# Kernel optimization log

Hardware: AMD Instinct MI355X
Metric: run time of the kernel (lower is better)

Reference implementation:

```python
import jax, jax.numpy as jnp
import numpy as np

PI = 3.141592653589793
IMG = 256           # img_size (input_resolution)
CONV = 2 * IMG      # conv_size for linear convolution
PITCH = 6.4e-6      # feature_size (m)
WAVELENGTH = 5.2e-7 # green channel, wavelength_list[1]
DISTANCE = 0.2      # distance_list[1] (m)
SCALE_OUT = 0.95    # scale_output


def make_H(n, pitch, wl, z):
    """Angular-spectrum transfer function, unshifted (fft) frequency order."""
    fx = np.fft.fftfreq(n, d=pitch).astype(np.float64)
    FX, FY = np.meshgrid(fx, fx, indexing='xy')
    fz2 = (1.0 / wl) ** 2 - FX ** 2 - FY ** 2
    prop = fz2 > 0
    kz = 2.0 * np.pi * np.sqrt(np.maximum(fz2, 0.0))
    H = np.exp(1j * kz * z) * prop
    return jnp.asarray(H.astype(np.complex64))


def setup_inputs() -> dict:
    key = jax.random.key(0)
    k1, k2, k3 = jax.random.split(key, 3)
    K, D = 512, 256
    z_e_x = jax.random.normal(k1, (16, D, 64, 64), dtype=jnp.float32)
    poh_dec = jax.random.normal(k2, (16, 1, IMG, IMG), dtype=jnp.float32)
    emb = jax.random.uniform(k3, (K, D), dtype=jnp.float32,
                             minval=-1.0 / K, maxval=1.0 / K)
    H = make_H(CONV, PITCH, WAVELENGTH, DISTANCE)
    return {"z_e_x": z_e_x, "poh_dec": poh_dec, "emb": emb, "H": H}


def vq_straight_through(z_e_x, emb):
    # z_e_x: [B, D, h, w] -> BHWC flatten [N, D]
    B, D, h, w = z_e_x.shape
    ze = jnp.transpose(z_e_x, (0, 2, 3, 1)).reshape(-1, D)
    # squared L2 distances to codebook [N, K]
    d2 = (jnp.sum(ze * ze, axis=1, keepdims=True)
          - 2.0 * ze @ emb.T
          + jnp.sum(emb * emb, axis=1))
    idx = jnp.argmin(d2, axis=1)                      # [N]
    zq = jnp.take(emb, idx, axis=0).reshape(B, h, w, D)
    z_q_x = jnp.transpose(zq, (0, 3, 1, 2))           # BCHW (grads -> emb)
    # straight-through: codebook detached, grad flows to z_e_x
    z_q_x_st = z_e_x + jax.lax.stop_gradient(z_q_x - z_e_x)
    return z_q_x_st, z_q_x


def recon_hologram(poh, H):
    # unit-amplitude phase-only field: exp(i*poh)
    field = jax.lax.complex(jnp.cos(poh), jnp.sin(poh))
    pad = (CONV - IMG) // 2
    padded = jnp.pad(field, ((0, 0), (0, 0), (pad, pad), (pad, pad)))  # zero pad
    u = jnp.fft.fft2(jnp.fft.ifftshift(padded, axes=(-2, -1)), norm='ortho')
    u = H * u
    u = jnp.fft.fftshift(jnp.fft.ifft2(u, norm='ortho'), axes=(-2, -1))
    u = u[..., pad:pad + IMG, pad:pad + IMG]          # center crop
    intensity = (jnp.abs(u) ** 2) * SCALE_OUT
    return jnp.sqrt(intensity)


def reference(z_e_x, poh_dec, emb, H):
    z_q_x_st, z_q_x = vq_straight_through(z_e_x, emb)
    # decoder (external VQGAN blocks) stands in as poh_dec; then Hardtanh(-pi, pi)
    poh = jnp.clip(poh_dec, -PI, PI)
    recon_img = recon_hologram(poh, H)
    return (poh, recon_img, z_e_x, z_q_x)
```

## Files before the change

kernel.cpp:

```cpp
#include <hip/hip_runtime.h>

#define PI_F 3.14159265358979323846f

typedef __attribute__((ext_vector_type(8))) _Float16 f16x8;
typedef __attribute__((ext_vector_type(4))) _Float16 f16x4;
typedef __attribute__((ext_vector_type(4))) float floatx4;
typedef __attribute__((ext_vector_type(4))) float f32x4;
typedef __attribute__((ext_vector_type(2))) float f32x2;

__device__ __forceinline__ void gload16(const void* src, void* dst) {
    __builtin_amdgcn_global_load_lds(
        (const __attribute__((address_space(1))) unsigned int*)src,
        (__attribute__((address_space(3))) unsigned int*)dst, 16, 0, 0);
}

__device__ __forceinline__ f32x4 ntload4(const float* p) {
    return __builtin_nontemporal_load((const f32x4*)p);
}
__device__ __forceinline__ void ntstore4(float* p, f32x4 v) {
    __builtin_nontemporal_store(v, (f32x4*)p);
}
__device__ __forceinline__ float2 ntload2(const float2* p) {
    return __builtin_bit_cast(float2, __builtin_nontemporal_load((const f32x2*)p));
}
__device__ __forceinline__ void ntstore2(float2* p, float2 v) {
    __builtin_nontemporal_store(__builtin_bit_cast(f32x2, v), (f32x2*)p);
}
__device__ __forceinline__ float ntload1(const float* p) {
    return __builtin_nontemporal_load(p);
}
__device__ __forceinline__ void ntstore1(float* p, float v) {
    __builtin_nontemporal_store(v, p);
}

__device__ __forceinline__ int swz(int p) { return p ^ ((p >> 5) & 15); }

__device__ __forceinline__ float2 cadd(float2 a, float2 b) {
    return make_float2(a.x + b.x, a.y + b.y);
}
__device__ __forceinline__ float2 csub(float2 a, float2 b) {
    return make_float2(a.x - b.x, a.y - b.y);
}
__device__ __forceinline__ float2 cmul(float2 a, float2 w) {
    return make_float2(a.x * w.x - a.y * w.y, a.x * w.y + a.y * w.x);
}
__device__ __forceinline__ float2 cmulc(float2 a, float2 w) {
    return make_float2(a.x * w.x + a.y * w.y, a.y * w.x - a.x * w.y);
}

template <int S>
__device__ __forceinline__ void dif_triple(float2* X, const float2* tw, int ss) {
    const int Q = 1 << (S - 2);
    int block = ss >> (S - 2);
    int j0 = ss & (Q - 1);
    int base = (block << (S + 1)) + j0;
    float2 v[8];
#pragma unroll
    for (int t = 0; t < 8; ++t) v[t] = X[swz(base + t * Q)];
#pragma unroll
    for (int t = 0; t < 4; ++t) {
        float2 w = tw[(j0 + t * Q) << (8 - S)];
        float2 a = v[t], b = v[t + 4];
        v[t] = cadd(a, b);
        v[t + 4] = cmul(csub(a, b), w);
    }
#pragma unroll
    for (int h = 0; h < 2; ++h)
#pragma unroll
        for (int t0 = 0; t0 < 2; ++t0) {
            int t = h * 4 + t0;
            float2 w = tw[(j0 + t0 * Q) << (9 - S)];
            float2 a = v[t], b = v[t + 2];
            v[t] = cadd(a, b);
            v[t + 2] = cmul(csub(a, b), w);
        }
    {
        float2 w = tw[j0 << (10 - S)];
#pragma unroll
        for (int t = 0; t < 8; t += 2) {
            float2 a = v[t], b = v[t + 1];
            v[t] = cadd(a, b);
            v[t + 1] = cmul(csub(a, b), w);
        }
    }
#pragma unroll
    for (int t = 0; t < 8; ++t) X[swz(base + t * Q)] = v[t];
}

template <int S>
__device__ __forceinline__ void dit_triple(float2* X, const float2* tw, int ss) {
    const int Q = 1 << (S - 2);
    int block = ss >> (S - 2);
    int j0 = ss & (Q - 1);
    int base = (block << (S + 1)) + j0;
    float2 v[8];
#pragma unroll
    for (int t = 0; t < 8; ++t) v[t] = X[swz(base + t * Q)];
    {
        float2 w = tw[j0 << (10 - S)];
#pragma unroll
        for (int t = 0; t < 8; t += 2) {
            float2 a = v[t], b = cmulc(v[t + 1], w);
            v[t] = cadd(a, b);
            v[t + 1] = csub(a, b);
        }
    }
#pragma unroll
    for (int h = 0; h < 2; ++h)
#pragma unroll
        for (int t0 = 0; t0 < 2; ++t0) {
            int t = h * 4 + t0;
            float2 w = tw[(j0 + t0 * Q) << (9 - S)];
            float2 a = v[t], b = cmulc(v[t + 2], w);
            v[t] = cadd(a, b);
            v[t + 2] = csub(a, b);
        }
#pragma unroll
    for (int t = 0; t < 4; ++t) {
        float2 w = tw[(j0 + t * Q) << (8 - S)];
        float2 a = v[t], b = cmulc(v[t + 4], w);
        v[t] = cadd(a, b);
        v[t + 4] = csub(a, b);
    }
#pragma unroll
    for (int t = 0; t < 8; ++t) X[swz(base + t * Q)] = v[t];
}

__global__ void k_init(float2* __restrict__ Hs, const float* __restrict__ emb,
                       _Float16* __restrict__ eh, float* __restrict__ eq) {
    __shared__ float red[4];
    int blk = blockIdx.x;
    if (blk < 1024) {
        int g = blk * 256 + threadIdx.x;
        int ybr = g >> 9, xbr = g & 511;
        int ky = __brev((unsigned)ybr) >> 23;
        int kx = __brev((unsigned)xbr) >> 23;
        double val = 1.0 / (512.0 * 6.4e-6);
        double fy = (double)((ky < 256) ? ky : ky - 512) * val;
        double fx = (double)((kx < 256) ? kx : kx - 512) * val;
        double iw = 1.0 / 5.2e-7;
        double px = fx * fx, py = fy * fy;
        double fz2 = (iw * iw - px) - py;
        float2 h = make_float2(0.f, 0.f);
        if (fz2 > 0.0) {
            double t = sqrt(fz2) * 0.2;
            double fr = t - floor(t);
            double sv, cv;
            sincospi(2.0 * fr, &sv, &cv);
            const double sc = 1.0 / 262144.0;
            h = make_float2((float)(cv * sc), (float)(sv * sc));
        }
        Hs[g] = h;
    } else {
        int k = blk - 1024;
        int t = threadIdx.x;
        float v = emb[k * 256 + t];
        eh[k * 256 + t] = (_Float16)v;
        float s = v * v;
        for (int off = 32; off; off >>= 1) s += __shfl_down(s, off);
        if ((t & 63) == 0) red[t >> 6] = s;
        __syncthreads();
        if (t == 0) eq[k] = red[0] + red[1] + red[2] + red[3];
    }
}

__global__ __launch_bounds__(256, 3) void k_vq(const float* __restrict__ ze,
                                               const _Float16* __restrict__ eh,
                                               const float* __restrict__ eq,
                                               int* __restrict__ idx,
                                               float* __restrict__ zeout) {
    __shared__ _Float16 B[2][4096];
    __shared__ _Float16 Ast[4][32][136];
    int tid = threadIdx.x;
    int lane = tid & 63, wave = tid >> 6;
    int n0 = blockIdx.x * 128 + wave * 32;
    int b = n0 >> 12;
    int s0 = n0 & 4095;
    int m = lane & 15;
    int q = lane >> 4;

    const _Float16* srcp = eh + m * 256 + (wave * 4 + q) * 8;

#define STAGE(kt_, buf_)  do {                                               \
        const _Float16* s_ = srcp + (kt_) * 4096;    \
        _Float16* d_ = &B[buf_][wave * 512];                                 \
        gload16(s_,       d_);                                               \
        gload16(s_ + 128, d_ + 2048);         \
    } while (0)

    STAGE(0, 0);

    const float* zb = ze + (size_t)b * (256 * 4096);
    float* zo = zeout ? zeout + (size_t)b * (256 * 4096) : nullptr;
    int g = lane >> 3;
    int s4 = lane & 7;
    f16x8 a[2][8];
#pragma unroll
    for (int half = 0; half < 2; ++half) {
#pragma unroll
        for (int c2 = 0; c2 < 4; ++c2) {
            int c = half * 4 + c2;
            float vv[4][4];
#pragma unroll
            for (int dd = 0; dd < 4; ++dd) {
                int d = c * 32 + g * 4 + dd;
                size_t off = (size_t)d * 4096 + s0 + s4 * 4;
                f32x4 t = ntload4(&zb[off]);
                if (zeout) ntstore4(&zo[off], t);
                vv[dd][0] = t.x; vv[dd][1] = t.y;
                vv[dd][2] = t.z; vv[dd][3] = t.w;
            }
#pragma unroll
            for (int i = 0; i < 4; ++i) {
                f16x4 p = {(_Float16)vv[0][i], (_Float16)vv[1][i],
                           (_Float16)vv[2][i], (_Float16)vv[3][i]};
                *(f16x4*)&Ast[wave][s4 * 4 + i][c2 * 32 + g * 4] = p;
            }
        }
#pragma unroll
        for (int c2 = 0; c2 < 4; ++c2)
#pragma unroll
            for (int T = 0; T < 2; ++T)
                a[T][half * 4 + c2] =
                    *(const f16x8*)&Ast[wave][T * 16 + m][c2 * 32 + q * 8];
    }
    __syncthreads();

    float best[2][4];
    int bidx[2][4];
#pragma unroll
    for (int T = 0; T < 2; ++T)
#pragma unroll
        for (int r = 0; r < 4; ++r) { best[T][r] = 3.4e38f; bidx[T][r] = 0x7fffffff; }

    int cur = 0;
    for (int kt = 0; kt < 32; ++kt) {
        if (kt < 31) STAGE(kt + 1, cur ^ 1);

        int kc = kt * 16 + m;
        float eqv = eq[kc];
        floatx4 acc0 = {0.f, 0.f, 0.f, 0.f};
        floatx4 acc1 = {0.f, 0.f, 0.f, 0.f};
        const _Float16* b0 = &B[cur][q * 128 + m * 8];
#pragma unroll
        for (int c = 0; c < 8; ++c) {
            f16x8 bb = *(const f16x8*)(b0 + c * 512);
            acc0 = __builtin_amdgcn_mfma_f32_16x16x32_f16(a[0][c], bb, acc0, 0, 0, 0);
            acc1 = __builtin_amdgcn_mfma_f32_16x16x32_f16(a[1][c], bb, acc1, 0, 0, 0);
        }
#pragma unroll
        for (int r = 0; r < 4; ++r) {
            float d0 = eqv - 2.0f * acc0[r];
            if (d0 < best[0][r]) { best[0][r] = d0; bidx[0][r] = kc; }
            float d1 = eqv - 2.0f * acc1[r];
            if (d1 < best[1][r]) { best[1][r] = d1; bidx[1][r] = kc; }
        }
        __syncthreads();
        cur ^= 1;
    }
#undef STAGE

#pragma unroll
    for (int T = 0; T < 2; ++T)
#pragma unroll
        for (int r = 0; r < 4; ++r) {
            float bv = best[T][r];
            int bi = bidx[T][r];
            for (int off = 1; off < 16; off <<= 1) {
                float ov = __shfl_xor(bv, off);
                int oi = __shfl_xor(bi, off);
                if (ov < bv || (ov == bv && oi < bi)) { bv = ov; bi = oi; }
            }
            if (m == 0) idx[n0 + T * 16 + q * 4 + r] = bi;
        }
}

__global__ __launch_bounds__(256) void k_zq(const float* __restrict__ emb,
                                            const int* __restrict__ idx,
                                            float* __restrict__ out4) {
    __shared__ float E[32 * 257];
    __shared__ int sidx[32];
    int tid = threadIdx.x;
    int blk = blockIdx.x;
    int b = blk >> 7;
    int s0 = (blk & 127) << 5;
    if (tid < 32) sidx[tid] = idx[(b << 12) + s0 + tid];
    __syncthreads();
#pragma unroll
    for (int i = 0; i < 32; ++i)
        E[i * 257 + tid] = emb[sidx[i] * 256 + tid];
    __syncthreads();
    float* ob = out4 + ((size_t)b << 20) + s0;
    int s_off = tid & 31, d0 = tid >> 5;
#pragma unroll
    for (int i2 = 0; i2 < 32; ++i2) {
        int d = d0 + (i2 << 3);
        ntstore1(&ob[((size_t)d << 12) + s_off], E[s_off * 257 + d]);
    }
}

__global__ void k_ze(const float* __restrict__ ze, float* __restrict__ out3) {
    size_t g = (size_t)blockIdx.x * 256 + threadIdx.x;
    ntstore4(&((float*)out3)[g * 4], ntload4(&((const float*)ze)[g * 4]));
}

__global__ __launch_bounds__(256) void k_fwd_rows(const float* __restrict__ poh_in,
                                                  float* __restrict__ poh_out,
                                                  float2* __restrict__ F) {
    __shared__ float2 Xs[4][512];
    __shared__ float2 tw[256];
    int tid = threadIdx.x;
    {
        float sv, cv;
        sincospif(-(float)tid * (1.0f / 256.0f), &sv, &cv);
        tw[tid] = make_float2(cv, sv);
    }
    __syncthreads();
    int wave = tid >> 6, lane = tid & 63;
    int b = blockIdx.x >> 6;
    int t = ((blockIdx.x & 63) << 2) + wave;
    int jy = (t < 128) ? t : t + 256;
    int ry = (t < 128) ? t + 128 : t - 128;
    float2* X = Xs[wave];

    const float* prow = poh_in + (b << 16) + (ry << 8);
    float* orow = poh_out + (b << 16) + (ry << 8);
#pragma unroll
    for (int c0 = 0; c0 < 256; c0 += 64) {
        int c = c0 + lane;
        float v = ntload1(&prow[c]);
        v = fminf(fmaxf(v, -PI_F), PI_F);
        ntstore1(&orow[c], v);
        float sv, cv;
        __sincosf(v, &sv, &cv);
        int jx = (c < 128) ? c + 384 : c - 128;
        X[swz(jx)] = make_float2(cv, sv);
    }
#pragma unroll
    for (int p0 = 128; p0 < 384; p0 += 64) X[swz(p0 + lane)] = make_float2(0.f, 0.f);

    dif_triple<8>(X, tw, lane);
    dif_triple<5>(X, tw, lane);
    dif_triple<2>(X, tw, lane);

    float2* Frow = F + ((size_t)(b * 512 + jy) << 9);
#pragma unroll
    for (int p0 = 0; p0 < 512; p0 += 64)
        ntstore2(&Frow[p0 + lane], X[swz(p0 + lane)]);
}

__global__ __launch_bounds__(256) void k_cols(float2* __restrict__ F,
                                              const float2* __restrict__ Hs) {
    __shared__ float2 X[8 * 514];
    __shared__ float2 tw[256];
    int tid = threadIdx.x;
    {
        float sv, cv;
        sincospif(-(float)tid * (1.0f / 256.0f), &sv, &cv);
        tw[tid] = make_float2(cv, sv);
    }
    int b = blockIdx.x >> 6;
    int jx0 = (blockIdx.x & 63) << 3;
    const size_t ibase = ((size_t)b << 18);

#pragma unroll
    for (int i0 = 0; i0 < 8 * 256; i0 += 256) {
        int ii = i0 + tid;
        int col = ii & 7, rr = ii >> 3;
        int jy = (rr < 128) ? rr : rr + 256;
        X[col * 514 + swz(jy)] = ntload2(&F[ibase + ((size_t)jy << 9) + jx0 + col]);
    }
#pragma unroll
    for (int i0 = 0; i0 < 8 * 256; i0 += 256) {
        int ii = i0 + tid;
        int col = ii & 7, rr = ii >> 3;
        X[col * 514 + swz(128 + rr)] = make_float2(0.f, 0.f);
    }
    __syncthreads();

    int wave = tid >> 6, lane = tid & 63;
    int colh = lane >> 5;
    int r = lane & 31;
    float2* Xc = X + (wave * 2 + colh) * 514;

    dif_triple<8>(Xc, tw, r);       dif_triple<8>(Xc, tw, 32 + r);
    dif_triple<5>(Xc, tw, r);       dif_triple<5>(Xc, tw, 32 + r);
    dif_triple<2>(Xc, tw, r);       dif_triple<2>(Xc, tw, 32 + r);

    {
        int gc = jx0 + wave * 2 + colh;
#pragma unroll
        for (int p0 = 0; p0 < 512; p0 += 32) {
            int p = p0 + r;
            float2 h = Hs[((size_t)p << 9) + gc];
            int qs = swz(p);
            Xc[qs] = cmul(Xc[qs], h);
        }
    }

    dit_triple<2>(Xc, tw, r);       dit_triple<2>(Xc, tw, 32 + r);
    dit_triple<5>(Xc, tw, r);       dit_triple<5>(Xc, tw, 32 + r);
    dit_triple<8>(Xc, tw, r);       dit_triple<8>(Xc, tw, 32 + r);

    __syncthreads();
#pragma unroll
    for (int i0 = 0; i0 < 8 * 256; i0 += 256) {
        int ii = i0 + tid;
        int col = ii & 7, rr = ii >> 3;
        int jy = (rr < 128) ? rr : rr + 256;
        ntstore2(&F[ibase + ((size_t)jy << 9) + jx0 + col],
                 X[col * 514 + swz(jy)]);
    }
}

__global__ __launch_bounds__(256) void k_inv_rows(const float2* __restrict__ F,
                                                  float* __restrict__ out2) {
    __shared__ float2 Xs[4][512];
    __shared__ float2 tw[256];
    int tid = threadIdx.x;
    {
        float sv, cv;
        sincospif(-(float)tid * (1.0f / 256.0f), &sv, &cv);
        tw[tid] = make_float2(cv, sv);
    }
    __syncthreads();
    int wave = tid >> 6, lane = tid & 63;
    int b = blockIdx.x >> 6;
    int t = ((blockIdx.x & 63) << 2) + wave;
    int jy = (t < 128) ? t : t + 256;
    int r = (t < 128) ? t + 128 : t - 128;
    float2* X = Xs[wave];

    const float2* Frow = F + ((size_t)(b * 512 + jy) << 9);
#pragma unroll
    for (int p0 = 0; p0 < 512; p0 += 64)
        X[swz(p0 + lane)] = ntload2(&Frow[p0 + lane]);

    dit_triple<2>(X, tw, lane);
    dit_triple<5>(X, tw, lane);
    dit_triple<8>(X, tw, lane);

    float* orow = out2 + (b << 16) + (r << 8);
    const float SC = 0.97467943448f;
#pragma unroll
    for (int c0 = 0; c0 < 256; c0 += 64) {
        int c = c0 + lane;
        int jx = (c < 128) ? c + 384 : c - 128;
        float2 u = X[swz(jx)];
        ntstore1(&orow[c], sqrtf(u.x * u.x + u.y * u.y) * SC);
    }
}

extern "C" void kernel_launch(void* const* d_in, const int* in_sizes, int n_in,
                              void* d_out, int out_size, void* d_ws, size_t ws_size,
                              hipStream_t stream) {
    const float* ze  = (const float*)d_in[0];
    const float* poh = (const float*)d_in[1];
    const float* emb = (const float*)d_in[2];

    float* out  = (float*)d_out;
    float* out1 = out;
    float* out2 = out + 1048576;
    float* out3 = out + 2097152;
    float* out4 = out + 18874368;

    const size_t WS_NEED = 262144 + 2048 + 262144 + 2097152;
    bool fused = (d_ws != nullptr) && (ws_size >= WS_NEED);
    char* base = fused ? (char*)d_ws : (char*)out3;
    _Float16* eh;
    float* eq;
    int* idxp;
    float2* Hs;
    if (fused) {
        eh   = (_Float16*)base;
        eq   = (float*)(base + 262144);
        idxp = (int*)(base + 264192);
        Hs   = (float2*)(base + 526336);
    } else {
        eh   = (_Float16*)base;
        eq   = (float*)(base + 262144);
        idxp = (int*)(base + 264192);
        Hs   = (float2*)(base + 1048576);
    }
    float2* F = (float2*)out4;

    k_init    <<<1536, 256, 0, stream>>>(Hs, emb, eh, eq);
    k_vq      <<<512, 256, 0, stream>>>(ze, eh, eq, idxp,
                                        fused ? out3 : (float*)nullptr);
    k_fwd_rows<<<1024, 256, 0, stream>>>(poh, out1, F);
    k_cols    <<<1024, 256, 0, stream>>>(F, Hs);
    k_inv_rows<<<1024, 256, 0, stream>>>(F, out2);
    k_zq      <<<2048, 256, 0, stream>>>(emb, idxp, out4);
    if (!fused)
        k_ze  <<<16384, 256, 0, stream>>>(ze, out3);
}
```

Before: 265.5 us.

## Merge VQ argmin and forward row FFT into one heterogeneous launch

Combines the VQ nearest-codebook kernel and the forward row FFT kernel into a single launch whose blocks branch by blockIdx: the first 512 blocks do VQ and the remaining 1024 do the row FFTs, sharing one raw shared-memory buffer. The intent is to run the MFMA-bound VQ work alongside the memory-bound FFT rows and to drop one kernel launch and its tail. The cost is that every block reserves the larger shared-memory footprint and the launch bounds of the VQ path, which may lower occupancy for the FFT blocks.

```diff
diff --git a/kernel.cpp b/kernel.cpp
--- a/kernel.cpp
+++ b/kernel.cpp
@@ -164,115 +164,162 @@
     }
 }
 
-__global__ __launch_bounds__(256, 3) void k_vq(const float* __restrict__ ze,
-                                               const _Float16* __restrict__ eh,
-                                               const float* __restrict__ eq,
-                                               int* __restrict__ idx,
-                                               float* __restrict__ zeout) {
-    __shared__ _Float16 B[2][4096];
-    __shared__ _Float16 Ast[4][32][136];
+__global__ __launch_bounds__(256, 3) void k_vq_fwd(
+        const float* __restrict__ ze, const _Float16* __restrict__ eh,
+        const float* __restrict__ eq, int* __restrict__ idx,
+        float* __restrict__ zeout,
+        const float* __restrict__ poh_in, float* __restrict__ poh_out,
+        float2* __restrict__ F) {
+    __shared__ __align__(16) char smem[51200];
     int tid = threadIdx.x;
     int lane = tid & 63, wave = tid >> 6;
-    int n0 = blockIdx.x * 128 + wave * 32;
-    int b = n0 >> 12;
-    int s0 = n0 & 4095;
-    int m = lane & 15;
-    int q = lane >> 4;
-
-    const _Float16* srcp = eh + m * 256 + (wave * 4 + q) * 8;
+
+    if (blockIdx.x < 512) {
+        _Float16* B = (_Float16*)smem;
+        _Float16* Ast = (_Float16*)(smem + 16384);
+        int n0 = blockIdx.x * 128 + wave * 32;
+        int b = n0 >> 12;
+        int s0 = n0 & 4095;
+        int m = lane & 15;
+        int q = lane >> 4;
+
+        const _Float16* srcp = eh + m * 256 + (wave * 4 + q) * 8;
 
 #define STAGE(kt_, buf_)  do {                                               \
         const _Float16* s_ = srcp + (kt_) * 4096;    \
-        _Float16* d_ = &B[buf_][wave * 512];                                 \
+        _Float16* d_ = B + (buf_) * 4096 + wave * 512;                       \
         gload16(s_,       d_);                                               \
         gload16(s_ + 128, d_ + 2048);         \
     } while (0)
 
-    STAGE(0, 0);
-
-    const float* zb = ze + (size_t)b * (256 * 4096);
-    float* zo = zeout ? zeout + (size_t)b * (256 * 4096) : nullptr;
-    int g = lane >> 3;
-    int s4 = lane & 7;
-    f16x8 a[2][8];
-#pragma unroll
-    for (int half = 0; half < 2; ++half) {
-#pragma unroll
-        for (int c2 = 0; c2 < 4; ++c2) {
-            int c = half * 4 + c2;
-            float vv[4][4];
-#pragma unroll
-            for (int dd = 0; dd < 4; ++dd) {
-                int d = c * 32 + g * 4 + dd;
-                size_t off = (size_t)d * 4096 + s0 + s4 * 4;
-                f32x4 t = ntload4(&zb[off]);
-                if (zeout) ntstore4(&zo[off], t);
-                vv[dd][0] = t.x; vv[dd][1] = t.y;
-                vv[dd][2] = t.z; vv[dd][3] = t.w;
+        STAGE(0, 0);
+
+        const float* zb = ze + (size_t)b * (256 * 4096);
+        float* zo = zeout ? zeout + (size_t)b * (256 * 4096) : nullptr;
+        int g = lane >> 3;
+        int s4 = lane & 7;
+        _Float16* Aw = Ast + wave * (32 * 136);
+        f16x8 a[2][8];
+#pragma unroll
+        for (int half = 0; half < 2; ++half) {
+#pragma unroll
+            for (int c2 = 0; c2 < 4; ++c2) {
+                int c = half * 4 + c2;
+                float vv[4][4];
+#pragma unroll
+                for (int dd = 0; dd < 4; ++dd) {
+                    int d = c * 32 + g * 4 + dd;
+                    size_t off = (size_t)d * 4096 + s0 + s4 * 4;
+                    f32x4 t = ntload4(&zb[off]);
+                    if (zeout) ntstore4(&zo[off], t);
+                    vv[dd][0] = t.x; vv[dd][1] = t.y;
+                    vv[dd][2] = t.z; vv[dd][3] = t.w;
+                }
+#pragma unroll
+                for (int i = 0; i < 4; ++i) {
+                    f16x4 p = {(_Float16)vv[0][i], (_Float16)vv[1][i],
+                               (_Float16)vv[2][i], (_Float16)vv[3][i]};
+                    *(f16x4*)&Aw[(s4 * 4 + i) * 136 + c2 * 32 + g * 4] = p;
+                }
             }
 #pragma unroll
-            for (int i = 0; i < 4; ++i) {
-                f16x4 p = {(_Float16)vv[0][i], (_Float16)vv[1][i],
-                           (_Float16)vv[2][i], (_Float16)vv[3][i]};
-                *(f16x4*)&Ast[wave][s4 * 4 + i][c2 * 32 + g * 4] = p;
+            for (int c2 = 0; c2 < 4; ++c2)
+#pragma unroll
+                for (int T = 0; T < 2; ++T)
+                    a[T][half * 4 + c2] =
+                        *(const f16x8*)&Aw[(T * 16 + m) * 136 + c2 * 32 + q * 8];
+        }
+        __syncthreads();
+
+        float best[2][4];
+        int bidx[2][4];
+#pragma unroll
+        for (int T = 0; T < 2; ++T)
+#pragma unroll
+            for (int r = 0; r < 4; ++r) { best[T][r] = 3.4e38f; bidx[T][r] = 0x7fffffff; }
+
+        int cur = 0;
+        for (int kt = 0; kt < 32; ++kt) {
+            if (kt < 31) STAGE(kt + 1, cur ^ 1);
+
+            int kc = kt * 16 + m;
+            float eqv = eq[kc];
+            floatx4 acc0 = {0.f, 0.f, 0.f, 0.f};
+            floatx4 acc1 = {0.f, 0.f, 0.f, 0.f};
+            const _Float16* b0 = B + cur * 4096 + q * 128 + m * 8;
+#pragma unroll
+            for (int c = 0; c < 8; ++c) {
+                f16x8 bb = *(const f16x8*)(b0 + c * 512);
+                acc0 = __builtin_amdgcn_mfma_f32_16x16x32_f16(a[0][c], bb, acc0, 0, 0, 0);
+                acc1 = __builtin_amdgcn_mfma_f32_16x16x32_f16(a[1][c], bb, acc1, 0, 0, 0);
             }
-        }
-#pragma unroll
-        for (int c2 = 0; c2 < 4; ++c2)
-#pragma unroll
-            for (int T = 0; T < 2; ++T)
-                a[T][half * 4 + c2] =
-                    *(const f16x8*)&Ast[wave][T * 16 + m][c2 * 32 + q * 8];
-    }
-    __syncthreads();
-
-    float best[2][4];
-    int bidx[2][4];
-#pragma unroll
-    for (int T = 0; T < 2; ++T)
-#pragma unroll
-        for (int r = 0; r < 4; ++r) { best[T][r] = 3.4e38f; bidx[T][r] = 0x7fffffff; }
-
-    int cur = 0;
-    for (int kt = 0; kt < 32; ++kt) {
-        if (kt < 31) STAGE(kt + 1, cur ^ 1);
-
-        int kc = kt * 16 + m;
-        float eqv = eq[kc];
-        floatx4 acc0 = {0.f, 0.f, 0.f, 0.f};
-        floatx4 acc1 = {0.f, 0.f, 0.f, 0.f};
-        const _Float16* b0 = &B[cur][q * 128 + m * 8];
-#pragma unroll
-        for (int c = 0; c < 8; ++c) {
-            f16x8 bb = *(const f16x8*)(b0 + c * 512);
-            acc0 = __builtin_amdgcn_mfma_f32_16x16x32_f16(a[0][c], bb, acc0, 0, 0, 0);
-            acc1 = __builtin_amdgcn_mfma_f32_16x16x32_f16(a[1][c], bb, acc1, 0, 0, 0);
-        }
-#pragma unroll
-        for (int r = 0; r < 4; ++r) {
-            float d0 = eqv - 2.0f * acc0[r];
-            if (d0 < best[0][r]) { best[0][r] = d0; bidx[0][r] = kc; }
-            float d1 = eqv - 2.0f * acc1[r];
-            if (d1 < best[1][r]) { best[1][r] = d1; bidx[1][r] = kc; }
+#pragma unroll
+            for (int r = 0; r < 4; ++r) {
+                float d0 = eqv - 2.0f * acc0[r];
+                if (d0 < best[0][r]) { best[0][r] = d0; bidx[0][r] = kc; }
+                float d1 = eqv - 2.0f * acc1[r];
+                if (d1 < best[1][r]) { best[1][r] = d1; bidx[1][r] = kc; }
+            }
+            __syncthreads();
+            cur ^= 1;
+        }
+#undef STAGE
+
+#pragma unroll
+        for (int T = 0; T < 2; ++T)
+#pragma unroll
+            for (int r = 0; r < 4; ++r) {
+                float bv = best[T][r];
+                int bi = bidx[T][r];
+                for (int off = 1; off < 16; off <<= 1) {
+                    float ov = __shfl_xor(bv, off);
+                    int oi = __shfl_xor(bi, off);
+                    if (ov < bv || (ov == bv && oi < bi)) { bv = ov; bi = oi; }
+                }
+                if (m == 0) idx[n0 + T * 16 + q * 4 + r] = bi;
+            }
+    } else {
+        float2* Xs = (float2*)smem;
+        float2* tw = (float2*)(smem + 16384);
+        int blk = blockIdx.x - 512;
+        {
+            float sv, cv;
+            sincospif(-(float)tid * (1.0f / 256.0f), &sv, &cv);
+            tw[tid] = make_float2(cv, sv);
         }
         __syncthreads();
-        cur ^= 1;
-    }
-#undef STAGE
-
-#pragma unroll
-    for (int T = 0; T < 2; ++T)
-#pragma unroll
-        for (int r = 0; r < 4; ++r) {
-            float bv = best[T][r];
-            int bi = bidx[T][r];
-            for (int off = 1; off < 16; off <<= 1) {
-                float ov = __shfl_xor(bv, off);
-                int oi = __shfl_xor(bi, off);
-                if (ov < bv || (ov == bv && oi < bi)) { bv = ov; bi = oi; }
-            }
-            if (m == 0) idx[n0 + T * 16 + q * 4 + r] = bi;
-        }
+        int b = blk >> 6;
+        int t = ((blk & 63) << 2) + wave;
+        int jy = (t < 128) ? t : t + 256;
+        int ry = (t < 128) ? t + 128 : t - 128;
+        float2* X = Xs + wave * 512;
+
+        const float* prow = poh_in + (b << 16) + (ry << 8);
+        float* orow = poh_out + (b << 16) + (ry << 8);
+#pragma unroll
+        for (int c0 = 0; c0 < 256; c0 += 64) {
+            int c = c0 + lane;
+            float v = ntload1(&prow[c]);
+            v = fminf(fmaxf(v, -PI_F), PI_F);
+            ntstore1(&orow[c], v);
+            float sv, cv;
+            __sincosf(v, &sv, &cv);
+            int jx = (c < 128) ? c + 384 : c - 128;
+            X[swz(jx)] = make_float2(cv, sv);
+        }
+#pragma unroll
+        for (int p0 = 128; p0 < 384; p0 += 64)
+            X[swz(p0 + lane)] = make_float2(0.f, 0.f);
+
+        dif_triple<8>(X, tw, lane);
+        dif_triple<5>(X, tw, lane);
+        dif_triple<2>(X, tw, lane);
+
+        float2* Frow = F + ((size_t)(b * 512 + jy) << 9);
+#pragma unroll
+        for (int p0 = 0; p0 < 512; p0 += 64)
+            ntstore2(&Frow[p0 + lane], X[swz(p0 + lane)]);
+    }
 }
 
 __global__ __launch_bounds__(256) void k_zq(const float* __restrict__ emb,
@@ -302,51 +349,6 @@
 __global__ void k_ze(const float* __restrict__ ze, float* __restrict__ out3) {
     size_t g = (size_t)blockIdx.x * 256 + threadIdx.x;
     ntstore4(&((float*)out3)[g * 4], ntload4(&((const float*)ze)[g * 4]));
-}
-
-__global__ __launch_bounds__(256) void k_fwd_rows(const float* __restrict__ poh_in,
-                                                  float* __restrict__ poh_out,
-                                                  float2* __restrict__ F) {
-    __shared__ float2 Xs[4][512];
-    __shared__ float2 tw[256];
-    int tid = threadIdx.x;
-    {
-        float sv, cv;
-        sincospif(-(float)tid * (1.0f / 256.0f), &sv, &cv);
-        tw[tid] = make_float2(cv, sv);
-    }
-    __syncthreads();
-    int wave = tid >> 6, lane = tid & 63;
-    int b = blockIdx.x >> 6;
-    int t = ((blockIdx.x & 63) << 2) + wave;
-    int jy = (t < 128) ? t : t + 256;
-    int ry = (t < 128) ? t + 128 : t - 128;
-    float2* X = Xs[wave];
-
-    const float* prow = poh_in + (b << 16) + (ry << 8);
-    float* orow = poh_out + (b << 16) + (ry << 8);
-#pragma unroll
-    for (int c0 = 0; c0 < 256; c0 += 64) {
-        int c = c0 + lane;
-        float v = ntload1(&prow[c]);
-        v = fminf(fmaxf(v, -PI_F), PI_F);
-        ntstore1(&orow[c], v);
-        float sv, cv;
-        __sincosf(v, &sv, &cv);
-        int jx = (c < 128) ? c + 384 : c - 128;
-        X[swz(jx)] = make_float2(cv, sv);
-    }
-#pragma unroll
-    for (int p0 = 128; p0 < 384; p0 += 64) X[swz(p0 + lane)] = make_float2(0.f, 0.f);
-
-    dif_triple<8>(X, tw, lane);
-    dif_triple<5>(X, tw, lane);
-    dif_triple<2>(X, tw, lane);
-
-    float2* Frow = F + ((size_t)(b * 512 + jy) << 9);
-#pragma unroll
-    for (int p0 = 0; p0 < 512; p0 += 64)
-        ntstore2(&Frow[p0 + lane], X[swz(p0 + lane)]);
 }
 
 __global__ __launch_bounds__(256) void k_cols(float2* __restrict__ F,
@@ -485,9 +487,9 @@
     float2* F = (float2*)out4;
 
     k_init    <<<1536, 256, 0, stream>>>(Hs, emb, eh, eq);
-    k_vq      <<<512, 256, 0, stream>>>(ze, eh, eq, idxp,
-                                        fused ? out3 : (float*)nullptr);
-    k_fwd_rows<<<1024, 256, 0, stream>>>(poh, out1, F);
+    k_vq_fwd  <<<1536, 256, 0, stream>>>(ze, eh, eq, idxp,
+                                         fused ? out3 : (float*)nullptr,
+                                         poh, out1, F);
     k_cols    <<<1024, 256, 0, stream>>>(F, Hs);
     k_inv_rows<<<1024, 256, 0, stream>>>(F, out2);
     k_zq      <<<2048, 256, 0, stream>>>(emb, idxp, out4);
```

After: 263.6 us. No clear change (-0.7%).
